# Kernel tuning notes

Hardware: AMD Instinct MI355X
Metric: run time of the kernel (lower is better)

Reference implementation:

```python
import jax, jax.numpy as jnp
import numpy as np

NUM_CLASSES = 1024
TAU = 1.0


def setup_inputs() -> dict:
    key = jax.random.key(0)
    k1, k2, k3 = jax.random.split(key, 3)
    N_s, N_q, D = 65536, 65536, 512
    z_support = jax.random.normal(k1, (N_s, D), dtype=jnp.float32)
    y_support = jax.random.randint(k2, (N_s,), 0, NUM_CLASSES, dtype=jnp.int64)
    z_query = jax.random.normal(k3, (N_q, D), dtype=jnp.float32)
    return {"z_support": z_support, "y_support": y_support, "z_query": z_query}


def reference(z_support, y_support, z_query):
    # Per-class mean prototypes via a single segment reduce.
    # (Assumes all classes 0..C-1 appear in y_support, so torch.unique remap is identity.)
    sums = jax.ops.segment_sum(z_support, y_support, num_segments=NUM_CLASSES)  # [C, D]
    counts = jax.ops.segment_sum(
        jnp.ones((z_support.shape[0],), dtype=z_support.dtype),
        y_support, num_segments=NUM_CLASSES)  # [C]
    protos = sums / jnp.maximum(counts, 1.0)[:, None]  # [C, D]

    # Pairwise squared euclidean: ||q||^2 + ||p||^2 - 2 q.p
    q_sq = jnp.sum(z_query * z_query, axis=-1, keepdims=True)          # [Nq, 1]
    p_sq = jnp.sum(protos * protos, axis=-1)[None, :]                  # [1, C]
    cross = jnp.einsum("nd,cd->nc", z_query, protos)                   # [Nq, C]
    dist = q_sq + p_sq - 2.0 * cross
    logits = -TAU * dist
    return logits
```

## Files before the change

### kernel.cpp

```cpp
#include <hip/hip_runtime.h>
#include <stdint.h>

#define C_CLASSES 1024
#define D_DIM     512
#define N_SUP     65536
#define N_QRY     65536
#define SLOTS     144

typedef float f32x4 __attribute__((ext_vector_type(4)));
typedef float f32x16v __attribute__((ext_vector_type(16)));
typedef short bf16x8 __attribute__((ext_vector_type(8)));
typedef unsigned short u16x4 __attribute__((ext_vector_type(4)));
typedef unsigned short u16x8 __attribute__((ext_vector_type(8)));

#define GLOBAL_AS __attribute__((address_space(1)))
#define LDS_AS    __attribute__((address_space(3)))

__device__ inline void async_copy16(const void* g, void* l) {
    __builtin_amdgcn_global_load_lds((const GLOBAL_AS void*)g, (LDS_AS void*)l, 16, 0, 0);
}

__device__ inline unsigned short f2bf(float f) {
    union { float f; unsigned int u; } x; x.f = f;
    unsigned int u = x.u;
    return (unsigned short)((u + 0x7fffu + ((u >> 16) & 1u)) >> 16);
}

__global__ void init_kernel(int* __restrict__ cursors) {
    cursors[threadIdx.x] = 0;
}

template<bool CONV>
__global__ __launch_bounds__(256) void qsq_conv_kernel(
    const float* __restrict__ zq, float* __restrict__ qsq,
    unsigned short* __restrict__ Abf,
    const int* __restrict__ ys, int* __restrict__ cursors,
    int* __restrict__ rowlist)
{
    if (blockIdx.x < N_SUP / 256) {
        int i = blockIdx.x * 256 + threadIdx.x;
        int c = ys[i];
        int slot = atomicAdd(&cursors[c], 1);
        if (slot < SLOTS) rowlist[c * SLOTS + slot] = i;
    }

    const int w    = threadIdx.x >> 6;
    const int lane = threadIdx.x & 63;
    const int row  = blockIdx.x * 4 + w;
    const f32x4* zp = (const f32x4*)(zq + (size_t)row * D_DIM);
    f32x4 a = zp[2 * lane];
    f32x4 b = zp[2 * lane + 1];
    if (CONV) {
        u16x8 p;
        p.s0 = f2bf(a.x); p.s1 = f2bf(a.y); p.s2 = f2bf(a.z); p.s3 = f2bf(a.w);
        p.s4 = f2bf(b.x); p.s5 = f2bf(b.y); p.s6 = f2bf(b.z); p.s7 = f2bf(b.w);
        *(u16x8*)(Abf + (size_t)row * D_DIM + lane * 8) = p;
    }
    float s = a.x*a.x + a.y*a.y + a.z*a.z + a.w*a.w
            + b.x*b.x + b.y*b.y + b.z*b.z + b.w*b.w;
    #pragma unroll
    for (int off = 32; off > 0; off >>= 1) s += __shfl_down(s, off, 64);
    if (lane == 0) qsq[row] = s;
}

__global__ __launch_bounds__(256) void proto_gather(
    const float* __restrict__ zs, const int* __restrict__ rowlist,
    const int* __restrict__ cursors, unsigned short* __restrict__ protos,
    float* __restrict__ psq)
{
    const int c    = blockIdx.x;
    const int tid  = threadIdx.x;
    const int w    = tid >> 6;
    const int lane = tid & 63;

    const int cnt = cursors[c];
    const int m   = cnt < SLOTS ? cnt : SLOTS;

    f32x4 s0 = {0.f, 0.f, 0.f, 0.f};
    f32x4 s1 = {0.f, 0.f, 0.f, 0.f};
    for (int j = w; j < m; j += 4) {
        int r = rowlist[c * SLOTS + j];
        const f32x4* zp = (const f32x4*)(zs + (size_t)r * D_DIM);
        s0 += zp[lane];
        s1 += zp[64 + lane];
    }

    __shared__ float sAcc[4][D_DIM];
    ((f32x4*)&sAcc[w][0])[lane]      = s0;
    ((f32x4*)&sAcc[w][0])[64 + lane] = s1;
    __syncthreads();

    float inv = 1.0f / fmaxf((float)cnt, 1.0f);
    int t2 = tid + 256;
    float p0 = (sAcc[0][tid] + sAcc[1][tid] + sAcc[2][tid] + sAcc[3][tid]) * inv;
    float p1 = (sAcc[0][t2]  + sAcc[1][t2]  + sAcc[2][t2]  + sAcc[3][t2])  * inv;
    protos[(size_t)c * D_DIM + tid] = f2bf(p0);
    protos[(size_t)c * D_DIM + t2]  = f2bf(p1);

    float ps = p0 * p0 + p1 * p1;
    #pragma unroll
    for (int off = 32; off > 0; off >>= 1) ps += __shfl_down(ps, off, 64);
    __shared__ float sPs[4];
    if (lane == 0) sPs[w] = ps;
    __syncthreads();
    if (tid == 0) psq[c] = sPs[0] + sPs[1] + sPs[2] + sPs[3];
}

template<bool FAST>
__global__ __launch_bounds__(256) void gemm_kernel(
    const float* __restrict__ A32, const unsigned short* __restrict__ Abf,
    const unsigned short* __restrict__ Bp,
    const float* __restrict__ qsq, const float* __restrict__ psq,
    float* __restrict__ out)
{
    constexpr int BM = 128, BN = 128, BK = 32, K = D_DIM, NN = C_CLASSES;
    __shared__ __align__(16) unsigned short shA[BM * BK];
    __shared__ __align__(16) unsigned short shB[BN * BK];

    const int tid  = threadIdx.x;
    const int lane = tid & 63;
    const int w    = tid >> 6;
    const int wm   = w >> 1, wn = w & 1;
    const int l31  = lane & 31, half = lane >> 5;
    const int mBase = blockIdx.y * BM;
    const int nBase = blockIdx.x * BN;

    const int srow = lane >> 2;
    const int sx   = lane & 3;
    const int scg  = (sx ^ ((srow >> 1) & 3)) * 8;

    f32x16v acc[2][2];
    #pragma unroll
    for (int i = 0; i < 2; i++)
        #pragma unroll
        for (int j = 0; j < 2; j++)
            acc[i][j] = (f32x16v)(0.0f);

    for (int k0 = 0; k0 < K; k0 += BK) {
        __syncthreads();
        if (FAST) {
            #pragma unroll
            for (int t = 0; t < 2; t++) {
                int ci = w * 2 + t;
                async_copy16(Abf + (size_t)(mBase + ci * 16 + srow) * K + k0 + scg,
                             &shA[ci * 16 * BK]);
                async_copy16(Bp  + (size_t)(nBase + ci * 16 + srow) * K + k0 + scg,
                             &shB[ci * 16 * BK]);
            }
        } else {
            #pragma unroll
            for (int t = 0; t < 2; t++) {
                int q = tid * 2 + t;
                int r = q >> 2;
                int x = q & 3;
                int cg = x ^ ((r >> 1) & 3);
                const float* src = A32 + (size_t)(mBase + r) * K + k0 + cg * 8;
                f32x4 v0 = *(const f32x4*)src;
                f32x4 v1 = *(const f32x4*)(src + 4);
                u16x8 p;
                p.s0 = f2bf(v0.x); p.s1 = f2bf(v0.y); p.s2 = f2bf(v0.z); p.s3 = f2bf(v0.w);
                p.s4 = f2bf(v1.x); p.s5 = f2bf(v1.y); p.s6 = f2bf(v1.z); p.s7 = f2bf(v1.w);
                *(u16x8*)&shA[r * BK + x * 8] = p;
            }
            #pragma unroll
            for (int t = 0; t < 2; t++) {
                int ci = w * 2 + t;
                async_copy16(Bp + (size_t)(nBase + ci * 16 + srow) * K + k0 + scg,
                             &shB[ci * 16 * BK]);
            }
        }
        __syncthreads();

        bf16x8 af[2][2], bfv[2][2];
        #pragma unroll
        for (int i = 0; i < 2; i++) {
            int ra = wm * 64 + i * 32 + l31;
            int ga = (ra >> 1) & 3;
            int rb = wn * 64 + i * 32 + l31;
            int gb = (rb >> 1) & 3;
            #pragma unroll
            for (int ks = 0; ks < 2; ks++) {
                int c = ks * 2 + half;
                af[i][ks]  = *(const bf16x8*)&shA[ra * BK + ((c ^ ga) * 8)];
                bfv[i][ks] = *(const bf16x8*)&shB[rb * BK + ((c ^ gb) * 8)];
            }
        }
        #pragma unroll
        for (int ks = 0; ks < 2; ks++)
            #pragma unroll
            for (int i = 0; i < 2; i++)
                #pragma unroll
                for (int j = 0; j < 2; j++)
                    acc[i][j] = __builtin_amdgcn_mfma_f32_32x32x16_bf16(
                        af[i][ks], bfv[j][ks], acc[i][j], 0, 0, 0);
    }

    const int rowb = mBase + wm * 64;
    const int colb = nBase + wn * 64;
    float pv[2];
    #pragma unroll
    for (int j = 0; j < 2; j++) pv[j] = psq[colb + j * 32 + l31];
    #pragma unroll
    for (int i = 0; i < 2; i++) {
        #pragma unroll
        for (int rg = 0; rg < 4; rg++) {
            int rbase = rowb + i * 32 + rg * 8 + half * 4;
            f32x4 qv = *(const f32x4*)&qsq[rbase];
            #pragma unroll
            for (int rr = 0; rr < 4; rr++) {
                int reg = rg * 4 + rr;
                size_t rowoff = (size_t)(rbase + rr) * NN;
                #pragma unroll
                for (int j = 0; j < 2; j++) {
                    out[rowoff + colb + j * 32 + l31] =
                        2.0f * acc[i][j][reg] - qv[rr] - pv[j];
                }
            }
        }
    }
}

extern "C" void kernel_launch(void* const* d_in, const int* in_sizes, int n_in,
                              void* d_out, int out_size, void* d_ws, size_t ws_size,
                              hipStream_t stream) {
    const float* zs = (const float*)d_in[0];
    const int*   ys = (const int*)d_in[1];
    const float* zq = (const float*)d_in[2];
    float* out = (float*)d_out;

    const size_t szAbf     = (size_t)N_QRY * D_DIM * 2;
    const size_t szProtos  = (size_t)C_CLASSES * D_DIM * 2;
    const size_t szQsq     = (size_t)N_QRY * 4;
    const size_t szRowlist = (size_t)C_CLASSES * SLOTS * 4;
    const size_t szPsq     = 4096;
    const size_t szCur     = 4096;

    const size_t needFast = szAbf + szProtos + szQsq + szRowlist + szPsq + szCur;
    const bool fast = ws_size >= needFast;

    char* ws = (char*)d_ws;
    unsigned short* Abf = (unsigned short*)ws;
    char* base = fast ? ws + szAbf : ws;
    unsigned short* protos = (unsigned short*)base;
    float* qsq  = (float*)(base + szProtos);
    int*   rowlist = (int*)(base + szProtos + szQsq);
    float* psq  = (float*)(base + szProtos + szQsq + szRowlist);
    int*   cursors = (int*)(base + szProtos + szQsq + szRowlist + szPsq);

    init_kernel<<<1, C_CLASSES, 0, stream>>>(cursors);
    if (fast)
        qsq_conv_kernel<true><<<N_QRY / 4, 256, 0, stream>>>(
            zq, qsq, Abf, ys, cursors, rowlist);
    else
        qsq_conv_kernel<false><<<N_QRY / 4, 256, 0, stream>>>(
            zq, qsq, nullptr, ys, cursors, rowlist);
    proto_gather<<<C_CLASSES, 256, 0, stream>>>(zs, rowlist, cursors, protos, psq);
    if (fast)
        gemm_kernel<true><<<dim3(C_CLASSES / 128, N_QRY / 128), 256, 0, stream>>>(
            nullptr, Abf, protos, qsq, psq, out);
    else
        gemm_kernel<false><<<dim3(C_CLASSES / 128, N_QRY / 128), 256, 0, stream>>>(
            zq, nullptr, protos, qsq, psq, out);
}
```

Baseline: 560.1 us.

## Double GEMM K-tile to 64 with new LDS swizzle and unroll proto gather

Raises the GEMM K-tile from 32 to 64. This halves the number of K iterations and their barrier pairs, and the LDS staging and XOR swizzle are reworked for 8 chunks per row. The proto gather kernel now stages its row indices in LDS and unrolls the accumulation loop by two, so more global loads are in flight at once. The cost is twice the LDS per block, which may lower occupancy, and more fragment registers.

```diff
diff --git a/kernel.cpp b/kernel.cpp
--- a/kernel.cpp
+++ b/kernel.cpp
@@ -76,10 +76,25 @@
     const int cnt = cursors[c];
     const int m   = cnt < SLOTS ? cnt : SLOTS;
 
+    __shared__ int sRows[SLOTS];
+    if (tid < m) sRows[tid] = rowlist[c * SLOTS + tid];
+    __syncthreads();
+
     f32x4 s0 = {0.f, 0.f, 0.f, 0.f};
     f32x4 s1 = {0.f, 0.f, 0.f, 0.f};
-    for (int j = w; j < m; j += 4) {
-        int r = rowlist[c * SLOTS + j];
+    int j = w;
+    for (; j + 4 < m; j += 8) {
+        int r0 = sRows[j];
+        int r1 = sRows[j + 4];
+        const f32x4* z0 = (const f32x4*)(zs + (size_t)r0 * D_DIM);
+        const f32x4* z1 = (const f32x4*)(zs + (size_t)r1 * D_DIM);
+        f32x4 a0 = z0[lane], a1 = z0[64 + lane];
+        f32x4 b0 = z1[lane], b1 = z1[64 + lane];
+        s0 += a0; s1 += a1;
+        s0 += b0; s1 += b1;
+    }
+    for (; j < m; j += 4) {
+        int r = sRows[j];
         const f32x4* zp = (const f32x4*)(zs + (size_t)r * D_DIM);
         s0 += zp[lane];
         s1 += zp[64 + lane];
@@ -113,7 +128,7 @@
     const float* __restrict__ qsq, const float* __restrict__ psq,
     float* __restrict__ out)
 {
-    constexpr int BM = 128, BN = 128, BK = 32, K = D_DIM, NN = C_CLASSES;
+    constexpr int BM = 128, BN = 128, BK = 64, K = D_DIM, NN = C_CLASSES;
     __shared__ __align__(16) unsigned short shA[BM * BK];
     __shared__ __align__(16) unsigned short shB[BN * BK];
 
@@ -125,9 +140,8 @@
     const int mBase = blockIdx.y * BM;
     const int nBase = blockIdx.x * BN;
 
-    const int srow = lane >> 2;
-    const int sx   = lane & 3;
-    const int scg  = (sx ^ ((srow >> 1) & 3)) * 8;
+    const int srow = lane >> 3;
+    const int scg  = ((lane & 7) ^ srow) * 8;
 
     f32x16v acc[2][2];
     #pragma unroll
@@ -140,20 +154,20 @@
         __syncthreads();
         if (FAST) {
             #pragma unroll
-            for (int t = 0; t < 2; t++) {
-                int ci = w * 2 + t;
-                async_copy16(Abf + (size_t)(mBase + ci * 16 + srow) * K + k0 + scg,
-                             &shA[ci * 16 * BK]);
-                async_copy16(Bp  + (size_t)(nBase + ci * 16 + srow) * K + k0 + scg,
-                             &shB[ci * 16 * BK]);
+            for (int t = 0; t < 4; t++) {
+                int g = w * 4 + t;
+                async_copy16(Abf + (size_t)(mBase + g * 8 + srow) * K + k0 + scg,
+                             &shA[g * 8 * BK]);
+                async_copy16(Bp  + (size_t)(nBase + g * 8 + srow) * K + k0 + scg,
+                             &shB[g * 8 * BK]);
             }
         } else {
             #pragma unroll
-            for (int t = 0; t < 2; t++) {
-                int q = tid * 2 + t;
-                int r = q >> 2;
-                int x = q & 3;
-                int cg = x ^ ((r >> 1) & 3);
+            for (int t = 0; t < 4; t++) {
+                int q = tid * 4 + t;
+                int r = q >> 3;
+                int x = q & 7;
+                int cg = x ^ (r & 7);
                 const float* src = A32 + (size_t)(mBase + r) * K + k0 + cg * 8;
                 f32x4 v0 = *(const f32x4*)src;
                 f32x4 v1 = *(const f32x4*)(src + 4);
@@ -163,30 +177,30 @@
                 *(u16x8*)&shA[r * BK + x * 8] = p;
             }
             #pragma unroll
-            for (int t = 0; t < 2; t++) {
-                int ci = w * 2 + t;
-                async_copy16(Bp + (size_t)(nBase + ci * 16 + srow) * K + k0 + scg,
-                             &shB[ci * 16 * BK]);
+            for (int t = 0; t < 4; t++) {
+                int g = w * 4 + t;
+                async_copy16(Bp + (size_t)(nBase + g * 8 + srow) * K + k0 + scg,
+                             &shB[g * 8 * BK]);
             }
         }
         __syncthreads();
 
-        bf16x8 af[2][2], bfv[2][2];
+        bf16x8 af[2][4], bfv[2][4];
         #pragma unroll
         for (int i = 0; i < 2; i++) {
             int ra = wm * 64 + i * 32 + l31;
-            int ga = (ra >> 1) & 3;
+            int ga = ra & 7;
             int rb = wn * 64 + i * 32 + l31;
-            int gb = (rb >> 1) & 3;
-            #pragma unroll
-            for (int ks = 0; ks < 2; ks++) {
+            int gb = rb & 7;
+            #pragma unroll
+            for (int ks = 0; ks < 4; ks++) {
                 int c = ks * 2 + half;
                 af[i][ks]  = *(const bf16x8*)&shA[ra * BK + ((c ^ ga) * 8)];
                 bfv[i][ks] = *(const bf16x8*)&shB[rb * BK + ((c ^ gb) * 8)];
             }
         }
         #pragma unroll
-        for (int ks = 0; ks < 2; ks++)
+        for (int ks = 0; ks < 4; ks++)
             #pragma unroll
             for (int i = 0; i < 2; i++)
                 #pragma unroll
```

New measurement: 544.8 us. 1.03x faster.
